# Kernel optimization log

Measured on AMD Instinct MI355X. Metric: run time of the kernel, lower is better.

The kernel has to match this reference:

```python
import jax, jax.numpy as jnp
import numpy as np
from jax.scipy.special import erf

N_POINTS = 5000
N_EVENTS = 1_000_000


def setup_inputs() -> dict:
    key = jax.random.key(0)
    k1, k2, k3, k4 = jax.random.split(key, 4)
    data_idx = jax.random.randint(k1, (N_EVENTS, 2), 0, N_POINTS, dtype=jnp.int32)
    data_t = jax.random.uniform(k2, (N_EVENTS,), dtype=jnp.float32) * 10.0
    # learned parameters, matching torch.rand(...)*0.5 init
    z0 = jax.random.uniform(k3, (N_POINTS, 2), dtype=jnp.float32) * 0.5
    v0 = jax.random.uniform(k4, (N_POINTS, 2), dtype=jnp.float32) * 0.5
    beta = jnp.ones((1, 1), dtype=jnp.float32)  # beta init = 1.0
    t0 = jnp.float32(0.0)
    tn = jnp.float32(10.0)
    return {"data_idx": data_idx, "data_t": data_t, "t0": t0, "tn": tn,
            "z0": z0, "v0": v0, "beta": beta}


def reference(data_idx, data_t, t0, tn, z0, v0, beta):
    b = beta[0, 0]
    # ---- event intensity: sum over events of (beta - ||z_i(t) - z_j(t)||^2)
    i = data_idx[:, 0]
    j = data_idx[:, 1]
    dz_e = (z0[i] - z0[j]) + (v0[i] - v0[j]) * data_t[:, None]  # [E,2]
    d_event = jnp.sum(dz_e * dz_e, axis=-1)                     # [E]
    n_events = data_t.shape[0]
    event_intensity = n_events * b - jnp.sum(d_event)

    # ---- non-event intensity: analytic integral over all node pairs i<j
    n = z0.shape[0]
    pi_idx, pj_idx = jnp.triu_indices(n, k=1)  # static node-pair list
    dz = z0[pi_idx] - z0[pj_idx]  # [P,2]
    dv = v0[pi_idx] - v0[pj_idx]  # [P,2]
    a2 = jnp.sum(dz * dz, axis=-1)       # ||dz||^2
    b2 = jnp.sum(dv * dv, axis=-1)       # ||dv||^2
    ab = jnp.sum(dz * dv, axis=-1)       # dz . dv
    bnorm = jnp.sqrt(b2)
    mu = ab / b2
    # integral_{t0}^{tn} exp(beta - ||dz + dv t||^2) dt
    #   = exp(beta - a2 + ab^2/b2) * sqrt(pi)/(2|dv|) * [erf(|dv|(tn+mu)) - erf(|dv|(t0+mu))]
    pref = jnp.exp(b - a2 + ab * mu) * (jnp.sqrt(jnp.pi) / (2.0 * bnorm))
    integral = pref * (erf(bnorm * (tn + mu)) - erf(bnorm * (t0 + mu)))
    non_event_intensity = jnp.sum(integral)

    log_likelihood = event_intensity - non_event_intensity
    return log_likelihood.reshape(1, 1)
```

## Files before the change

kernel.cpp:

```cpp
#include <hip/hip_runtime.h>
#include <math.h>


#define NBLK 4096
#define NTHR 256

__global__ void pack_kernel(const float* __restrict__ z0,
                            const float* __restrict__ v0,
                            float4* __restrict__ pts, int n_pts) {
    int p = blockIdx.x * blockDim.x + threadIdx.x;
    if (p < n_pts)
        pts[p] = make_float4(z0[2 * p], z0[2 * p + 1], v0[2 * p], v0[2 * p + 1]);
}

__device__ __forceinline__ float fast_exp(float x) {
    return __builtin_amdgcn_exp2f(x * 1.4426950408889634f);
}

__device__ __forceinline__ float fast_erf(float x) {
    float ax = fabsf(x);
    float t = __builtin_amdgcn_rcpf(fmaf(0.3275911f, ax, 1.0f));
    float p = fmaf(t, fmaf(t, fmaf(t, fmaf(t, 1.061405429f, -1.453152027f),
                                   1.421413741f), -0.284496736f), 0.254829592f);
    float y = fmaf(-(p * t), fast_exp(-ax * ax), 1.0f);
    return copysignf(y, x);
}

__global__ __launch_bounds__(256) void cvm_main_kernel(
    const int2* __restrict__ idx, const float* __restrict__ t,
    const float4* __restrict__ pts,
    const float* __restrict__ t0p, const float* __restrict__ tnp,
    const float* __restrict__ betap,
    int n_events, int n_pts, double* __restrict__ partials) {

    const float b  = betap[0];
    const float t0 = t0p[0];
    const float tn = tnp[0];
    const int tid = blockIdx.x * blockDim.x + threadIdx.x;
    const int nthreads = gridDim.x * blockDim.x;

    float local = 0.0f;

    for (int e = tid; e < n_events; e += nthreads) {
        int2 ij  = idx[e];
        float te = t[e];
        float4 pi = pts[ij.x];
        float4 pj = pts[ij.y];
        float dx = (pi.x - pj.x) + (pi.z - pj.z) * te;
        float dy = (pi.y - pj.y) + (pi.w - pj.w) * te;
        local = fmaf(dx, dx, fmaf(dy, dy, local));
    }

    const long long P = (long long)n_pts * (n_pts - 1) / 2;
    const int n_waves = nthreads >> 6;
    const int wave = tid >> 6;
    const int lane = threadIdx.x & 63;
    const long long per = (P + n_waves - 1) / n_waves;
    const long long kend = min((long long)(wave + 1) * per, P);
    long long k = (long long)wave * per + lane;

    const float spi2 = 0.88622692545275801365f;
    if (k < kend) {
        double nn = 2.0 * n_pts - 1.0;
        int i = (int)((nn - sqrt(fmax(nn * nn - 8.0 * (double)k, 0.0))) * 0.5);
        if (i < 0) i = 0;
        if (i > n_pts - 2) i = n_pts - 2;
        while ((long long)(i + 1) * (2LL * n_pts - i - 2) / 2 <= k) ++i;
        while ((long long)i * (2LL * n_pts - i - 1) / 2 > k) --i;
        int j = i + 1 + (int)(k - (long long)i * (2LL * n_pts - i - 1) / 2);

        float4 pi = pts[i];
        while (true) {
            float4 pj = pts[j];
            float dzx = pi.x - pj.x, dzy = pi.y - pj.y;
            float dvx = pi.z - pj.z, dvy = pi.w - pj.w;
            float a2 = fmaf(dzx, dzx, dzy * dzy);
            float b2 = fmaf(dvx, dvx, dvy * dvy);
            float ab = fmaf(dzx, dvx, dzy * dvy);
            float r   = __builtin_amdgcn_rsqf(b2);
            float rb2 = r * r;
            float mu  = ab * rb2;
            float e   = b - a2 + ab * mu;
            float pref = fast_exp(e) * (spi2 * r);
            float bnorm = b2 * r;
            float x1 = bnorm * (tn + mu);
            float x0 = bnorm * (t0 + mu);
            local = fmaf(pref, fast_erf(x1) - fast_erf(x0), local);

            k += 64;
            if (k >= kend) break;
            j += 64;
            if (j >= n_pts) {
                do { int over = j - n_pts; ++i; j = i + 1 + over; } while (j >= n_pts);
                pi = pts[i];
            }
        }
    }

    double v = (double)local;
    #pragma unroll
    for (int off = 32; off > 0; off >>= 1) v += __shfl_down(v, off, 64);
    __shared__ double wsum[4];
    if ((threadIdx.x & 63) == 0) wsum[threadIdx.x >> 6] = v;
    __syncthreads();
    if (threadIdx.x == 0)
        partials[blockIdx.x] = wsum[0] + wsum[1] + wsum[2] + wsum[3];
}

__global__ void finish_kernel(const double* __restrict__ partials, int nblk,
                              const float* __restrict__ betap,
                              float* __restrict__ out, int n_events) {
    double v = 0.0;
    for (int i = threadIdx.x; i < nblk; i += blockDim.x) v += partials[i];
    #pragma unroll
    for (int off = 32; off > 0; off >>= 1) v += __shfl_down(v, off, 64);
    __shared__ double wsum[4];
    if ((threadIdx.x & 63) == 0) wsum[threadIdx.x >> 6] = v;
    __syncthreads();
    if (threadIdx.x == 0)
        out[0] = (float)((double)n_events * (double)betap[0] -
                         (wsum[0] + wsum[1] + wsum[2] + wsum[3]));
}

extern "C" void kernel_launch(void* const* d_in, const int* in_sizes, int n_in,
                              void* d_out, int out_size, void* d_ws, size_t ws_size,
                              hipStream_t stream) {
    const int2*  idx  = (const int2*)d_in[0];
    const float* t    = (const float*)d_in[1];
    const float* t0   = (const float*)d_in[2];
    const float* tn   = (const float*)d_in[3];
    const float* z0   = (const float*)d_in[4];
    const float* v0   = (const float*)d_in[5];
    const float* beta = (const float*)d_in[6];
    const int n_events = in_sizes[1];
    const int n_pts    = in_sizes[4] / 2;

    double* partials = (double*)d_ws;
    float4* pts = (float4*)((char*)d_ws + NBLK * sizeof(double));

    pack_kernel<<<(n_pts + NTHR - 1) / NTHR, NTHR, 0, stream>>>(z0, v0, pts, n_pts);
    cvm_main_kernel<<<NBLK, NTHR, 0, stream>>>(idx, t, pts, t0, tn, beta,
                                               n_events, n_pts, partials);
    finish_kernel<<<1, NTHR, 0, stream>>>(partials, NBLK, beta,
                                          (float*)d_out, n_events);
}
```

Measured before the change: 102.3 us.

## Fold exp into erf terms, process two pairs per lane, fuse final reduction

The erf difference is rewritten algebraically so that exp(e) is folded into each erf tail, as exp2(e - x^2), which removes the separate prefactor exp and its multiply, with a jump term added when the interval crosses zero. Each lane now handles two pair streams A and B in a v2-style layout to raise instruction-level parallelism. The separate finish kernel is replaced by a last-block reduction that uses an atomic counter reset in the pack kernel, saving one launch. The cost is more decode work per lane and added complexity in the pair-advance logic, and the jump term adds a numerical-edge risk.

```diff
diff --git a/kernel.cpp b/kernel.cpp
--- a/kernel.cpp
+++ b/kernel.cpp
@@ -1,45 +1,73 @@
 #include <hip/hip_runtime.h>
 #include <math.h>
-
 
 #define NBLK 4096
 #define NTHR 256
 
+
+typedef float v2 __attribute__((ext_vector_type(2)));
+
+__device__ __forceinline__ v2 vfma2(v2 a, v2 b, v2 c) {
+    v2 r; r.x = fmaf(a.x, b.x, c.x); r.y = fmaf(a.y, b.y, c.y); return r;
+}
+
 __global__ void pack_kernel(const float* __restrict__ z0,
                             const float* __restrict__ v0,
-                            float4* __restrict__ pts, int n_pts) {
+                            float4* __restrict__ pts,
+                            unsigned int* __restrict__ counter, int n_pts) {
     int p = blockIdx.x * blockDim.x + threadIdx.x;
     if (p < n_pts)
         pts[p] = make_float4(z0[2 * p], z0[2 * p + 1], v0[2 * p], v0[2 * p + 1]);
+    if (p == 0) *counter = 0u;
 }
 
-__device__ __forceinline__ float fast_exp(float x) {
-    return __builtin_amdgcn_exp2f(x * 1.4426950408889634f);
+__device__ __forceinline__ float erf_term(float x, float eL) {
+    const float L2E = 1.4426950408889634f;
+    float ax = fabsf(x);
+    float tt = __builtin_amdgcn_rcpf(fmaf(0.3275911f, ax, 1.0f));
+    float P = tt * fmaf(tt, fmaf(tt, fmaf(tt, fmaf(tt, 1.061405429f, -1.453152027f),
+                        1.421413741f), -0.284496736f), 0.254829592f);
+    float arg = fmaf(x * L2E, -x, eL);
+    float PE = P * __builtin_amdgcn_exp2f(arg);
+    return copysignf(PE, x);
 }
 
-__device__ __forceinline__ float fast_erf(float x) {
-    float ax = fabsf(x);
-    float t = __builtin_amdgcn_rcpf(fmaf(0.3275911f, ax, 1.0f));
-    float p = fmaf(t, fmaf(t, fmaf(t, fmaf(t, 1.061405429f, -1.453152027f),
-                                   1.421413741f), -0.284496736f), 0.254829592f);
-    float y = fmaf(-(p * t), fast_exp(-ax * ax), 1.0f);
-    return copysignf(y, x);
+__device__ __forceinline__ void decode_k(long long k, int n, int& oi, int& oj) {
+    double nn = 2.0 * n - 1.0;
+    int i = (int)((nn - sqrt(fmax(nn * nn - 8.0 * (double)k, 0.0))) * 0.5);
+    i = max(0, min(i, n - 2));
+    while ((long long)(i + 1) * (2LL * n - i - 2) / 2 <= k) ++i;
+    while ((long long)i * (2LL * n - i - 1) / 2 > k) --i;
+    oi = i;
+    oj = i + 1 + (int)(k - (long long)i * (2LL * n - i - 1) / 2);
 }
 
-__global__ __launch_bounds__(256) void cvm_main_kernel(
+__device__ __forceinline__ void advance(int& i, int& j, int n, int step) {
+    j += step;
+    while (j >= n) {
+        if (i >= n - 2) { i = n - 2; j = n - 1; break; }
+        int over = j - n;
+        ++i;
+        j = i + 1 + over;
+    }
+}
+
+__global__ __launch_bounds__(NTHR) void cvm_main_kernel(
     const int2* __restrict__ idx, const float* __restrict__ t,
     const float4* __restrict__ pts,
     const float* __restrict__ t0p, const float* __restrict__ tnp,
     const float* __restrict__ betap,
-    int n_events, int n_pts, double* __restrict__ partials) {
+    int n_events, int n_pts,
+    double* __restrict__ partials, unsigned int* __restrict__ counter,
+    float* __restrict__ out) {
 
     const float b  = betap[0];
     const float t0 = t0p[0];
     const float tn = tnp[0];
-    const int tid = blockIdx.x * blockDim.x + threadIdx.x;
-    const int nthreads = gridDim.x * blockDim.x;
+    const int tid = blockIdx.x * NTHR + threadIdx.x;
+    const int nthreads = gridDim.x * NTHR;
 
-    float local = 0.0f;
+    v2 acc = {0.f, 0.f};
 
     for (int e = tid; e < n_events; e += nthreads) {
         int2 ij  = idx[e];
@@ -48,7 +76,7 @@
         float4 pj = pts[ij.y];
         float dx = (pi.x - pj.x) + (pi.z - pj.z) * te;
         float dy = (pi.y - pj.y) + (pi.w - pj.w) * te;
-        local = fmaf(dx, dx, fmaf(dy, dy, local));
+        acc.x = fmaf(dx, dx, fmaf(dy, dy, acc.x));
     }
 
     const long long P = (long long)n_pts * (n_pts - 1) / 2;
@@ -56,70 +84,88 @@
     const int wave = tid >> 6;
     const int lane = threadIdx.x & 63;
     const long long per = (P + n_waves - 1) / n_waves;
-    const long long kend = min((long long)(wave + 1) * per, P);
-    long long k = (long long)wave * per + lane;
+    const long long k0 = (long long)wave * per;
+    const long long kend = (k0 + per < P) ? (k0 + per) : P;
 
-    const float spi2 = 0.88622692545275801365f;
-    if (k < kend) {
-        double nn = 2.0 * n_pts - 1.0;
-        int i = (int)((nn - sqrt(fmax(nn * nn - 8.0 * (double)k, 0.0))) * 0.5);
-        if (i < 0) i = 0;
-        if (i > n_pts - 2) i = n_pts - 2;
-        while ((long long)(i + 1) * (2LL * n_pts - i - 2) / 2 <= k) ++i;
-        while ((long long)i * (2LL * n_pts - i - 1) / 2 > k) --i;
-        int j = i + 1 + (int)(k - (long long)i * (2LL * n_pts - i - 1) / 2);
+    const float SPI2 = 0.88622692545275801365f;
+    const float L2E  = 1.4426950408889634f;
 
-        float4 pi = pts[i];
-        while (true) {
-            float4 pj = pts[j];
-            float dzx = pi.x - pj.x, dzy = pi.y - pj.y;
-            float dvx = pi.z - pj.z, dvy = pi.w - pj.w;
-            float a2 = fmaf(dzx, dzx, dzy * dzy);
-            float b2 = fmaf(dvx, dvx, dvy * dvy);
-            float ab = fmaf(dzx, dvx, dzy * dvy);
-            float r   = __builtin_amdgcn_rsqf(b2);
-            float rb2 = r * r;
-            float mu  = ab * rb2;
-            float e   = b - a2 + ab * mu;
-            float pref = fast_exp(e) * (spi2 * r);
-            float bnorm = b2 * r;
-            float x1 = bnorm * (tn + mu);
-            float x0 = bnorm * (t0 + mu);
-            local = fmaf(pref, fast_erf(x1) - fast_erf(x0), local);
+    long long kA = k0 + lane;
+    if (kA < kend) {
+        int iA, jA, iB, jB;
+        decode_k(kA, n_pts, iA, jA);
+        long long kB = kA + 64;
+        decode_k((kB < P) ? kB : (P - 1), n_pts, iB, jB);
 
-            k += 64;
-            if (k >= kend) break;
-            j += 64;
-            if (j >= n_pts) {
-                do { int over = j - n_pts; ++i; j = i + 1 + over; } while (j >= n_pts);
-                pi = pts[i];
-            }
+        #pragma unroll 2
+        for (; kA < kend; kA += 128) {
+            bool validB = (kA + 64) < kend;
+            float4 PiA = pts[iA], PjA = pts[jA];
+            float4 PiB = pts[iB], PjB = pts[jB];
+
+            v2 dzx = {PiA.x - PjA.x, PiB.x - PjB.x};
+            v2 dzy = {PiA.y - PjA.y, PiB.y - PjB.y};
+            v2 dvx = {PiA.z - PjA.z, PiB.z - PjB.z};
+            v2 dvy = {PiA.w - PjA.w, PiB.w - PjB.w};
+
+            v2 a2 = vfma2(dzx, dzx, dzy * dzy);
+            v2 b2 = vfma2(dvx, dvx, dvy * dvy);
+            v2 ab = vfma2(dzx, dvx, dzy * dvy);
+            v2 r;  r.x = __builtin_amdgcn_rsqf(b2.x); r.y = __builtin_amdgcn_rsqf(b2.y);
+            v2 mu = ab * (r * r);
+            v2 bma2 = {b - a2.x, b - a2.y};
+            v2 e0 = vfma2(ab, mu, bma2);
+            v2 eL = e0 * L2E;
+            v2 bn = b2 * r;
+            v2 tnmu = {tn + mu.x, tn + mu.y};
+            v2 t0mu = {t0 + mu.x, t0 + mu.y};
+            v2 x1 = bn * tnmu;
+            v2 x0 = bn * t0mu;
+
+            v2 pe1; pe1.x = erf_term(x1.x, eL.x); pe1.y = erf_term(x1.y, eL.y);
+            v2 pe0; pe0.x = erf_term(x0.x, eL.x); pe0.y = erf_term(x0.y, eL.y);
+
+            v2 E0; E0.x = __builtin_amdgcn_exp2f(eL.x); E0.y = __builtin_amdgcn_exp2f(eL.y);
+            float jx = (x0.x < 0.f && x1.x >= 0.f) ? 2.f * E0.x : 0.f;
+            float jy = (x0.y < 0.f && x1.y >= 0.f) ? 2.f * E0.y : 0.f;
+
+            v2 sum = {jx + pe0.x - pe1.x, jy + pe0.y - pe1.y};
+            if (!validB) sum.y = 0.f;
+            v2 w = r * SPI2;
+            acc = vfma2(w, sum, acc);
+
+            advance(iA, jA, n_pts, 128);
+            advance(iB, jB, n_pts, 128);
         }
     }
 
-    double v = (double)local;
+    double v = (double)acc.x + (double)acc.y;
     #pragma unroll
     for (int off = 32; off > 0; off >>= 1) v += __shfl_down(v, off, 64);
     __shared__ double wsum[4];
+    __shared__ bool is_last;
     if ((threadIdx.x & 63) == 0) wsum[threadIdx.x >> 6] = v;
     __syncthreads();
-    if (threadIdx.x == 0)
+    if (threadIdx.x == 0) {
         partials[blockIdx.x] = wsum[0] + wsum[1] + wsum[2] + wsum[3];
-}
+        __threadfence();
+        unsigned int old = atomicAdd(counter, 1u);
+        is_last = (old == (unsigned int)(gridDim.x - 1));
+    }
+    __syncthreads();
 
-__global__ void finish_kernel(const double* __restrict__ partials, int nblk,
-                              const float* __restrict__ betap,
-                              float* __restrict__ out, int n_events) {
-    double v = 0.0;
-    for (int i = threadIdx.x; i < nblk; i += blockDim.x) v += partials[i];
-    #pragma unroll
-    for (int off = 32; off > 0; off >>= 1) v += __shfl_down(v, off, 64);
-    __shared__ double wsum[4];
-    if ((threadIdx.x & 63) == 0) wsum[threadIdx.x >> 6] = v;
-    __syncthreads();
-    if (threadIdx.x == 0)
-        out[0] = (float)((double)n_events * (double)betap[0] -
-                         (wsum[0] + wsum[1] + wsum[2] + wsum[3]));
+    if (is_last) {
+        __threadfence();
+        double s = 0.0;
+        for (int i = threadIdx.x; i < NBLK; i += NTHR) s += partials[i];
+        #pragma unroll
+        for (int off = 32; off > 0; off >>= 1) s += __shfl_down(s, off, 64);
+        if ((threadIdx.x & 63) == 0) wsum[threadIdx.x >> 6] = s;
+        __syncthreads();
+        if (threadIdx.x == 0)
+            out[0] = (float)((double)n_events * (double)betap[0] -
+                             (wsum[0] + wsum[1] + wsum[2] + wsum[3]));
+    }
 }
 
 extern "C" void kernel_launch(void* const* d_in, const int* in_sizes, int n_in,
@@ -136,11 +182,12 @@
     const int n_pts    = in_sizes[4] / 2;
 
     double* partials = (double*)d_ws;
-    float4* pts = (float4*)((char*)d_ws + NBLK * sizeof(double));
+    unsigned int* counter = (unsigned int*)((char*)d_ws + NBLK * sizeof(double));
+    float4* pts = (float4*)((char*)d_ws + NBLK * sizeof(double) + 16);
 
-    pack_kernel<<<(n_pts + NTHR - 1) / NTHR, NTHR, 0, stream>>>(z0, v0, pts, n_pts);
+    pack_kernel<<<(n_pts + NTHR - 1) / NTHR, NTHR, 0, stream>>>(z0, v0, pts,
+                                                                counter, n_pts);
     cvm_main_kernel<<<NBLK, NTHR, 0, stream>>>(idx, t, pts, t0, tn, beta,
-                                               n_events, n_pts, partials);
-    finish_kernel<<<1, NTHR, 0, stream>>>(partials, NBLK, beta,
-                                          (float*)d_out, n_events);
+                                               n_events, n_pts, partials,
+                                               counter, (float*)d_out);
 }
```

Result: slower. 237.8 us (+132.4%).
